# Kernel optimization log

Hardware: AMD Instinct MI355X
Metric: run time of the kernel (lower is better)

## Reference

```python
import math
import jax, jax.numpy as jnp
import numpy as np

B, L, D_MODEL = 2, 2048, 768
H = 12            # num_heads == num_key_value_heads
FEAT = 16         # feature_dim
HEAD_DIM = D_MODEL // H  # 64


def taylor_exp(x):
    """Taylor-exp feature map: phi(x) = [1, x/rrd, (x (x) x)/(sqrt(2)*rd)].
    x: [..., d] -> [..., 1 + d + d^2]"""
    d = x.shape[-1]
    rd = math.sqrt(d)
    rrd = math.sqrt(rd)
    r2 = math.sqrt(2.0)
    x2 = (x[..., :, None] * x[..., None, :]).reshape(*x.shape[:-1], d * d) / r2
    ones = jnp.ones(x.shape[:-1] + (1,), dtype=x.dtype)
    return jnp.concatenate([ones, x / rrd, x2 / rd], axis=-1)


def setup_inputs() -> dict:
    key = jax.random.key(0)
    k1, k2, k3, k4, k5 = jax.random.split(key, 5)
    s = 0.02
    return {
        "hidden_states": jax.random.normal(k1, (B, L, D_MODEL), jnp.float32),
        "Wq": jax.random.normal(k2, (H * FEAT, D_MODEL), jnp.float32) * s,
        "Wk": jax.random.normal(k3, (H * FEAT, D_MODEL), jnp.float32) * s,
        "Wv": jax.random.normal(k4, (D_MODEL, D_MODEL), jnp.float32) * s,
        "Wo": jax.random.normal(k5, (D_MODEL, D_MODEL), jnp.float32) * s,
    }


def reference(hidden_states, Wq, Wk, Wv, Wo):
    b, l, d = hidden_states.shape
    # projections (torch Linear, no bias): y = x @ W.T
    q = jnp.einsum('bld,fd->blf', hidden_states, Wq).reshape(b, l, H, FEAT).transpose(0, 2, 1, 3)
    k = jnp.einsum('bld,fd->blf', hidden_states, Wk).reshape(b, l, H, FEAT).transpose(0, 2, 1, 3)
    v = jnp.einsum('bld,fd->blf', hidden_states, Wv).reshape(b, l, H, HEAD_DIM).transpose(0, 2, 1, 3)

    q = taylor_exp(q)   # [b,h,l,Dexp]
    k = taylor_exp(k)   # k_enc == k (forward clones k), v_enc == v

    # denominator: k_enc.sum over seq + causal cumsum of k
    k_state = jnp.sum(k, axis=2, keepdims=True) + jnp.cumsum(k, axis=2)  # [b,h,l,Dexp]
    z = 1.0 / jnp.sum(q * k_state, axis=-1)                              # [b,h,l]

    # quadratic scores; y1 uses causal (tril) mask, y2 uses full scores with same k,v
    A = jnp.einsum('bhnd,bhmd->bhnm', q, k)                              # [b,h,l,l]
    causal = jnp.tril(jnp.ones((l, l), dtype=A.dtype))
    A_total = A * causal + A                                             # tril(A) + A
    y = jnp.einsum('bhnm,bhme->bhne', A_total, v) * z[..., None]         # [b,h,l,e]

    out = y.transpose(0, 2, 1, 3).reshape(b, l, H * HEAD_DIM)
    return jnp.einsum('blf,df->bld', out, Wo)
```

## Files before the change

kernel.cpp:

```cpp
#include <hip/hip_runtime.h>

typedef unsigned short ushortT;
typedef __bf16 bf16x8 __attribute__((ext_vector_type(8)));
typedef float f32x4 __attribute__((ext_vector_type(4)));

#define BB   2
#define LL   2048
#define DM   768
#define HH   12
#define FT   16
#define HD   64
#define DEXP 273
#define CH   128
#define NC   16
#define NBH  24
#define NBLK 384
#define C2f  0.17677669529663687f
#define KH   768
#define KP   1536
#define SLAB_US   4096
#define SPK_BLK_US 36864
#define SPK_BLK_B  73728

__device__ __forceinline__ void split_bf16(float x, ushortT& hi, ushortT& lo) {
  unsigned b = __float_as_uint(x);
  unsigned r = b + 0x7FFFu + ((b >> 16) & 1u);
  hi = (ushortT)(r >> 16);
  float hf = __uint_as_float((unsigned)hi << 16);
  lo = (ushortT)(__float_as_uint(x - hf) >> 16);
}

__global__ __launch_bounds__(256) void pack_a(const float* __restrict__ X,
                                              ushortT* __restrict__ Xh,
                                              int total4) {
  int g = blockIdx.x * 256 + threadIdx.x;
  if (g >= total4) return;
  int m = g / 192, k4 = (g % 192) * 4;
  float4 v = *(const float4*)(X + (size_t)m * 768 + k4);
  ushortT h[4], l[4];
  split_bf16(v.x, h[0], l[0]);
  split_bf16(v.y, h[1], l[1]);
  split_bf16(v.z, h[2], l[2]);
  split_bf16(v.w, h[3], l[3]);
  ushortT* p = Xh + (size_t)m * KP + k4;
  *(ushort4*)p = *(ushort4*)h;
  *(ushort4*)(p + KH) = *(ushort4*)l;
}

__global__ __launch_bounds__(256) void pack_w(const float* __restrict__ W0,
                                              const float* __restrict__ W1,
                                              const float* __restrict__ W2,
                                              int n1, int n2,
                                              ushortT* __restrict__ Wh,
                                              int total4) {
  int g = blockIdx.x * 256 + threadIdx.x;
  if (g >= total4) return;
  int n = g / 192, k4 = (g % 192) * 4;
  const float* src = (n < n1 ? W0 + (size_t)n * 768
                    : n < n2 ? W1 + (size_t)(n - n1) * 768
                             : W2 + (size_t)(n - n2) * 768);
  float4 v = *(const float4*)(src + k4);
  ushortT h[4], l[4];
  split_bf16(v.x, h[0], l[0]);
  split_bf16(v.y, h[1], l[1]);
  split_bf16(v.z, h[2], l[2]);
  split_bf16(v.w, h[3], l[3]);
  ushortT* p = Wh + (size_t)n * KP + k4;
  *(ushort4*)p = *(ushort4*)h;
  *(ushort4*)(p + KH) = *(ushort4*)l;
}

typedef const __attribute__((address_space(1))) unsigned gq_t;
typedef __attribute__((address_space(3))) unsigned lq_t;
__device__ __forceinline__ void gload_lds16(const ushortT* g, ushortT* l) {
  __builtin_amdgcn_global_load_lds((gq_t*)g, (lq_t*)l, 16, 0, 0);
}

__global__ __launch_bounds__(256) void mfma_gemm(const ushortT* __restrict__ A,
                                                 const ushortT* __restrict__ B,
                                                 float* __restrict__ Y, int ldy,
                                                 int ntiles) {
  __shared__ ushortT sAh[128 * 32], sAl[128 * 32], sBh[64 * 32], sBl[64 * 32];
  const int blk = blockIdx.x;
  const int xcd = blk & 7, slot = blk >> 3;
  const int mtp = gridDim.x / (8 * ntiles);
  const int mt = xcd * mtp + slot / ntiles;
  const int nt = slot % ntiles;
  const int bm = mt * 128, bn = nt * 64;
  const int tid = threadIdx.x, wave = tid >> 6, lane = tid & 63;
  const int srow = lane >> 2, schk = (lane & 3) * 8;
  const ushortT* gsrc;
  ushortT* lb;
  int iters;
  switch (wave) {
    case 0:  gsrc = A + (size_t)(bm + srow) * KP + schk;      lb = sAh; iters = 8; break;
    case 1:  gsrc = A + (size_t)(bm + srow) * KP + KH + schk; lb = sAl; iters = 8; break;
    case 2:  gsrc = B + (size_t)(bn + srow) * KP + schk;      lb = sBh; iters = 4; break;
    default: gsrc = B + (size_t)(bn + srow) * KP + KH + schk; lb = sBl; iters = 4; break;
  }
  const int wm = (wave & 1) * 64, wn = (wave >> 1) * 32;
  const int fr = lane & 15, quad = lane >> 4;
  f32x4 acc[4][2] = {};
  for (int k0 = 0; k0 < KH; k0 += 32) {
    __syncthreads();
    for (int it = 0; it < iters; it++)
      gload_lds16(gsrc + k0 + (size_t)it * 16 * KP, lb + it * 512);
    __syncthreads();
    bf16x8 ah[4], al[4], bh2[2], bl2[2];
#pragma unroll
    for (int mi = 0; mi < 4; mi++) {
      ah[mi] = *(const bf16x8*)&sAh[(wm + mi * 16 + fr) * 32 + quad * 8];
      al[mi] = *(const bf16x8*)&sAl[(wm + mi * 16 + fr) * 32 + quad * 8];
    }
#pragma unroll
    for (int ni = 0; ni < 2; ni++) {
      bh2[ni] = *(const bf16x8*)&sBh[(wn + ni * 16 + fr) * 32 + quad * 8];
      bl2[ni] = *(const bf16x8*)&sBl[(wn + ni * 16 + fr) * 32 + quad * 8];
    }
#pragma unroll
    for (int mi = 0; mi < 4; mi++)
#pragma unroll
      for (int ni = 0; ni < 2; ni++) {
        acc[mi][ni] = __builtin_amdgcn_mfma_f32_16x16x32_bf16(ah[mi], bh2[ni], acc[mi][ni], 0, 0, 0);
        acc[mi][ni] = __builtin_amdgcn_mfma_f32_16x16x32_bf16(ah[mi], bl2[ni], acc[mi][ni], 0, 0, 0);
        acc[mi][ni] = __builtin_amdgcn_mfma_f32_16x16x32_bf16(al[mi], bh2[ni], acc[mi][ni], 0, 0, 0);
      }
  }
  const int orow = quad * 4;
#pragma unroll
  for (int mi = 0; mi < 4; mi++)
#pragma unroll
    for (int ni = 0; ni < 2; ni++) {
      float* yp = Y + (size_t)(bm + wm + mi * 16 + orow) * ldy + bn + wn + ni * 16 + fr;
#pragma unroll
      for (int r = 0; r < 4; r++) yp[(size_t)r * ldy] = acc[mi][ni][r];
    }
}

__global__ __launch_bounds__(256, 2) void chunk_sum_kernel(
    const float* __restrict__ qkv, ushortT* __restrict__ Spk,
    float* __restrict__ csk) {
  const int blk = blockIdx.x;
  const int bh = blk >> 4, c = blk & 15;
  const int b = bh / HH, h = bh % HH;
  __shared__ float kT[16][128];
  __shared__ ushortT phiA[288][72];
  __shared__ ushortT Vt[64][72];
  const float* base = qkv + (size_t)(b * LL + c * CH) * 1152;
  const int tid = threadIdx.x;
  const int wave = tid >> 6, lane = tid & 63;
  const int fr = lane & 15, quad = lane >> 4;
  for (int idx = tid; idx < 512; idx += 256) {
    int m = idx >> 2, i4 = (idx & 3) * 4;
    float4 k4 = *(const float4*)&base[(size_t)m * 1152 + 192 + h * 16 + i4];
    kT[i4 + 0][m] = k4.x; kT[i4 + 1][m] = k4.y;
    kT[i4 + 2][m] = k4.z; kT[i4 + 3][m] = k4.w;
  }
  const int wm2 = (wave & 1) * 144, wn2 = (wave >> 1) * 32;
  f32x4 acc[9][2] = {};
  __syncthreads();
#pragma unroll 1
  for (int s = 0; s < 4; s++) {
    const int m0 = s * 32;
    if (s) __syncthreads();
    for (int idx = tid; idx < 512; idx += 256) {
      int m = m0 + (idx >> 4), e4 = (idx & 15) * 4;
      float4 v4 = *(const float4*)&base[(size_t)m * 1152 + 384 + h * 64 + e4];
      ushortT hh[4], ll[4];
      split_bf16(v4.x, hh[0], ll[0]); split_bf16(v4.y, hh[1], ll[1]);
      split_bf16(v4.z, hh[2], ll[2]); split_bf16(v4.w, hh[3], ll[3]);
      const int mi2 = m - m0;
#pragma unroll
      for (int j = 0; j < 4; j++) {
        Vt[e4 + j][mi2] = hh[j];
        Vt[e4 + j][32 + mi2] = ll[j];
      }
    }
    for (int rr = tid; rr < 288; rr += 256) {
      const int f = rr;
      const float* pa = (f >= 17) ? kT[(f - 17) >> 4] : (f >= 1 ? kT[f - 1] : kT[0]);
      const float* pb = (f >= 17) ? kT[(f - 17) & 15] : kT[0];
      const float sc = (f == 0) ? 1.0f : (f < 17 ? 0.5f : C2f);
      const bool quadf = (f >= 17);
      const bool valid = (f < DEXP);
      ushortT hrow[32], lrow[32];
#pragma unroll
      for (int g = 0; g < 8; g++) {
        float4 a4 = *(const float4*)&pa[m0 + g * 4];
        float4 b4 = *(const float4*)&pb[m0 + g * 4];
        float v0, v1, v2, v3;
        if (f == 0) {
          v0 = v1 = v2 = v3 = 1.0f;
        } else if (!quadf) {
          v0 = sc * a4.x; v1 = sc * a4.y; v2 = sc * a4.z; v3 = sc * a4.w;
        } else {
          v0 = sc * a4.x * b4.x; v1 = sc * a4.y * b4.y;
          v2 = sc * a4.z * b4.z; v3 = sc * a4.w * b4.w;
        }
        if (!valid) { v0 = v1 = v2 = v3 = 0.0f; }
        split_bf16(v0, hrow[g * 4 + 0], lrow[g * 4 + 0]);
        split_bf16(v1, hrow[g * 4 + 1], lrow[g * 4 + 1]);
        split_bf16(v2, hrow[g * 4 + 2], lrow[g * 4 + 2]);
        split_bf16(v3, hrow[g * 4 + 3], lrow[g * 4 + 3]);
      }
      *(uint4*)&phiA[f][0] = *(uint4*)&hrow[0];
      *(uint4*)&phiA[f][8] = *(uint4*)&hrow[8];
      *(uint4*)&phiA[f][16] = *(uint4*)&hrow[16];
      *(uint4*)&phiA[f][24] = *(uint4*)&hrow[24];
      *(uint4*)&phiA[f][32] = *(uint4*)&lrow[0];
      *(uint4*)&phiA[f][40] = *(uint4*)&lrow[8];
      *(uint4*)&phiA[f][48] = *(uint4*)&lrow[16];
      *(uint4*)&phiA[f][56] = *(uint4*)&lrow[24];
    }
    __syncthreads();
    bf16x8 bhf[2], blf[2];
#pragma unroll
    for (int ni = 0; ni < 2; ni++) {
      bhf[ni] = *(const bf16x8*)&Vt[wn2 + ni * 16 + fr][quad * 8];
      blf[ni] = *(const bf16x8*)&Vt[wn2 + ni * 16 + fr][32 + quad * 8];
    }
#pragma unroll
    for (int mi = 0; mi < 9; mi++) {
      bf16x8 ah = *(const bf16x8*)&phiA[wm2 + mi * 16 + fr][quad * 8];
      bf16x8 al = *(const bf16x8*)&phiA[wm2 + mi * 16 + fr][32 + quad * 8];
#pragma unroll
      for (int ni = 0; ni < 2; ni++) {
        acc[mi][ni] = __builtin_amdgcn_mfma_f32_16x16x32_bf16(ah, bhf[ni], acc[mi][ni], 0, 0, 0);
        acc[mi][ni] = __builtin_amdgcn_mfma_f32_16x16x32_bf16(ah, blf[ni], acc[mi][ni], 0, 0, 0);
        acc[mi][ni] = __builtin_amdgcn_mfma_f32_16x16x32_bf16(al, bhf[ni], acc[mi][ni], 0, 0, 0);
      }
    }
  }
  for (int f = tid; f < DEXP; f += 256) {
    float sum = 0.0f;
    if (f == 0) {
      sum = (float)CH;
    } else if (f < 17) {
      const float* p = kT[f - 1];
      for (int m = 0; m < CH; m += 4) {
        float4 x = *(const float4*)&p[m];
        sum += x.x + x.y + x.z + x.w;
      }
      sum *= 0.5f;
    } else {
      const float* pa2 = kT[(f - 17) >> 4];
      const float* pb2 = kT[(f - 17) & 15];
      for (int m = 0; m < CH; m += 4) {
        float4 x = *(const float4*)&pa2[m];
        float4 y = *(const float4*)&pb2[m];
        sum += x.x * y.x + x.y * y.y + x.z * y.z + x.w * y.w;
      }
      sum *= C2f;
    }
    csk[(size_t)blk * DEXP + f] = sum;
  }
  __syncthreads();
  ushortT* stage = &phiA[0][0];
  ushortT* Sp = Spk + (size_t)blk * SPK_BLK_US;
#pragma unroll 1
  for (int sl = 0; sl < 9; sl++) {
    if (sl) __syncthreads();
#pragma unroll
    for (int mi = 0; mi < 9; mi++) {
      const int fb = wm2 + mi * 16;
      if ((fb >> 5) == sl) {
        const int fi0 = (fb & 31) + quad * 4;
        const int gh = fi0 >> 3;
        const int inner = (fi0 << 1) & 15;
#pragma unroll
        for (int ni = 0; ni < 2; ni++) {
          const int e = wn2 + ni * 16 + fr;
          const int es = (e & 7) << 4;
          ushortT hh2[4], ll2[4];
#pragma unroll
          for (int r = 0; r < 4; r++) split_bf16(acc[mi][ni][r], hh2[r], ll2[r]);
          char* rowp = (char*)stage + e * 128;
          *(ushort4*)(rowp + ((gh << 4) ^ es) + inner) = *(ushort4*)hh2;
          *(ushort4*)(rowp + (((gh + 4) << 4) ^ es) + inner) = *(ushort4*)ll2;
        }
      }
    }
    __syncthreads();
    uint4* gdst = (uint4*)(Sp + (size_t)sl * SLAB_US);
    const uint4* lsrc = (const uint4*)stage;
    gdst[tid] = lsrc[tid];
    gdst[tid + 256] = lsrc[tid + 256];
  }
}

__global__ __launch_bounds__(256) void prefix_kernel(ushortT* __restrict__ Spk,
                                                     float* __restrict__ csk) {
  const int gid = blockIdx.x * 256 + threadIdx.x;
  const int totS = NBH * 4608;
  if (gid < totS) {
    const int bh = gid / 4608;
    const int rem = gid % 4608;
    const int slab = rem >> 9;
    const int e = (rem >> 3) & 63;
    const int wp = rem & 7;
    const int es = (e & 7) << 4;
    const unsigned off_h = e * 128 + ((((wp >> 1)) << 4) ^ es) + ((wp & 1) << 3);
    const unsigned off_l = e * 128 + ((((wp >> 1) + 4) << 4) ^ es) + ((wp & 1) << 3);
    char* base = (char*)Spk + (size_t)bh * NC * SPK_BLK_B + slab * 8192;
    float r0[NC], r1[NC], r2[NC], r3[NC];
    float t0 = 0.f, t1 = 0.f, t2 = 0.f, t3 = 0.f;
#pragma unroll
    for (int cc = 0; cc < NC; cc++) {
      const char* p = base + (size_t)cc * SPK_BLK_B;
      ushort4 hw = *(const ushort4*)(p + off_h);
      ushort4 lw = *(const ushort4*)(p + off_l);
      r0[cc] = __uint_as_float((unsigned)hw.x << 16) + __uint_as_float((unsigned)lw.x << 16);
      r1[cc] = __uint_as_float((unsigned)hw.y << 16) + __uint_as_float((unsigned)lw.y << 16);
      r2[cc] = __uint_as_float((unsigned)hw.z << 16) + __uint_as_float((unsigned)lw.z << 16);
      r3[cc] = __uint_as_float((unsigned)hw.w << 16) + __uint_as_float((unsigned)lw.w << 16);
      t0 += r0[cc]; t1 += r1[cc]; t2 += r2[cc]; t3 += r3[cc];
    }
    float u0 = 0.f, u1 = 0.f, u2 = 0.f, u3 = 0.f;
#pragma unroll
    for (int cc = 0; cc < NC; cc++) {
      ushort4 hw, lw;
      split_bf16(u0 + t0, hw.x, lw.x);
      split_bf16(u1 + t1, hw.y, lw.y);
      split_bf16(u2 + t2, hw.z, lw.z);
      split_bf16(u3 + t3, hw.w, lw.w);
      char* p = base + (size_t)cc * SPK_BLK_B;
      *(ushort4*)(p + off_h) = hw;
      *(ushort4*)(p + off_l) = lw;
      u0 += r0[cc]; u1 += r1[cc]; u2 += r2[cc]; u3 += r3[cc];
    }
  } else {
    const int g2 = gid - totS;
    if (g2 < NBH * DEXP) {
      const int bh = g2 / DEXP;
      const int f = g2 % DEXP;
      float r[NC];
      float tot = 0.0f;
#pragma unroll
      for (int cc = 0; cc < NC; cc++) {
        r[cc] = csk[(size_t)(bh * NC + cc) * DEXP + f];
        tot += r[cc];
      }
      float run = 0.0f;
#pragma unroll
      for (int cc = 0; cc < NC; cc++) {
        csk[(size_t)(bh * NC + cc) * DEXP + f] = run + tot;
        run += r[cc];
      }
    }
  }
}

__global__ __launch_bounds__(256, 2) void fused_out(
    const float* __restrict__ qkv, const ushortT* __restrict__ Spk,
    const float* __restrict__ csk, ushortT* __restrict__ Ahat) {
  const int blk = blockIdx.x;
  const int bh = blk >> 4, c = blk & 15;
  const int b = bh / HH, h = bh % HH;
  __shared__ ushortT phiA[128][72];
  __shared__ ushortT GtD[2][4096];
  __shared__ ushortT qA1[128][40];
  __shared__ ushortT qA2[128][40];
  __shared__ ushortT kB[32][40];
  __shared__ ushortT onesB[16][72];
  __shared__ float dred[128][2];
  __shared__ float zl[128];
  const int tid = threadIdx.x;
  const int wv = tid >> 6, lane = tid & 63;
  const int fr = lane & 15, quad = lane >> 4;
  const int prow = tid >> 1, phalf = tid & 1;
  const float* base = qkv + (size_t)(b * LL + c * CH) * 1152;
  const float* qrow = base + (size_t)prow * 1152 + h * 16;
  const ushortT* Gp = Spk + (size_t)blk * SPK_BLK_US;
  float qr[16];
#pragma unroll
  for (int i = 0; i < 4; i++) {
    float4 v = *(const float4*)(qrow + i * 4);
    qr[i * 4 + 0] = v.x; qr[i * 4 + 1] = v.y;
    qr[i * 4 + 2] = v.z; qr[i * 4 + 3] = v.w;
  }
  {
    const ushortT* s0 = Gp + wv * 1024 + lane * 8;
    gload_lds16(s0, &GtD[0][wv * 1024]);
    gload_lds16(s0 + 512, &GtD[0][wv * 1024 + 512]);
  }
  {
    ushortT qh[16], ql[16];
#pragma unroll
    for (int i = 0; i < 16; i++) split_bf16(qr[i], qh[i], ql[i]);
    *(uint4*)&qA1[prow][phalf * 16] = *(uint4*)&qh[0];
    *(uint4*)&qA1[prow][phalf * 16 + 8] = *(uint4*)&qh[8];
    *(uint4*)&qA2[prow][phalf * 16] = *(uint4*)&ql[0];
    *(uint4*)&qA2[prow][phalf * 16 + 8] = *(uint4*)&ql[8];
  }
  for (int idx = tid; idx < 16 * 64; idx += 256) {
    int row = idx >> 6, k = idx & 63;
    onesB[row][k] = (row == 0 && k < 32) ? (ushortT)0x3F80 : (ushortT)0;
  }
  const float* gkp = csk + (size_t)blk * DEXP;
  f32x4 acc[2][5] = {};
  float dacc = 0.0f;
#pragma unroll 1
  for (int s = 0; s < 9; s++) {
    __syncthreads();
    const int f0 = s * 32;
    float gkv[16];
#pragma unroll
    for (int j = 0; j < 16; j++) {
      const int f = f0 + phalf * 16 + j;
      gkv[j] = (f < DEXP) ? gkp[f] : 0.0f;
    }
    __builtin_amdgcn_sched_barrier(0);
    if (s < 8) {
      const ushortT* src = Gp + (s + 1) * SLAB_US + wv * 1024 + lane * 8;
      gload_lds16(src, &GtD[(s + 1) & 1][wv * 1024]);
      gload_lds16(src + 512, &GtD[(s + 1) & 1][wv * 1024 + 512]);
    }
    {
      ushortT h16[16], l16[16];
#pragma unroll
      for (int j = 0; j < 16; j++) {
        const int f = f0 + phalf * 16 + j;
        float v;
        if (f == 0) v = 1.0f;
        else if (f < 17) v = 0.5f * qr[f - 1];
        else if (f < DEXP) {
          const int ii = f - 17;
          v = C2f * qr[ii >> 4] * qr[ii & 15];
        } else v = 0.0f;
        dacc += v * gkv[j];
        split_bf16(v, h16[j], l16[j]);
      }
      *(uint4*)&phiA[prow][phalf * 16] = *(uint4*)&h16[0];
      *(uint4*)&phiA[prow][phalf * 16 + 8] = *(uint4*)&h16[8];
      *(uint4*)&phiA[prow][32 + phalf * 16] = *(uint4*)&l16[0];
      *(uint4*)&phiA[prow][32 + phalf * 16 + 8] = *(uint4*)&l16[8];
    }
    bf16x8 ah[2], al[2];
#pragma unroll
    for (int mi = 0; mi < 2; mi++) {
      ah[mi] = *(const bf16x8*)&phiA[wv * 32 + mi * 16 + fr][quad * 8];
      al[mi] = *(const bf16x8*)&phiA[wv * 32 + mi * 16 + fr][32 + quad * 8];
    }
    const char* gt = (const char*)&GtD[s & 1][0];
    const int sw = (fr & 7) << 4;
#pragma unroll
    for (int ni = 0; ni < 4; ni++) {
      const int rb = (ni * 16 + fr) * 128;
      bf16x8 bh2 = *(const bf16x8*)(gt + rb + ((quad * 16) ^ sw));
      bf16x8 bl2 = *(const bf16x8*)(gt + rb + ((64 + quad * 16) ^ sw));
#pragma unroll
      for (int mi = 0; mi < 2; mi++) {
        acc[mi][ni] = __builtin_amdgcn_mfma_f32_16x16x32_bf16(ah[mi], bh2, acc[mi][ni], 0, 0, 0);
        acc[mi][ni] = __builtin_amdgcn_mfma_f32_16x16x32_bf16(ah[mi], bl2, acc[mi][ni], 0, 0, 0);
        acc[mi][ni] = __builtin_amdgcn_mfma_f32_16x16x32_bf16(al[mi], bh2, acc[mi][ni], 0, 0, 0);
      }
    }
  }
  dred[prow][phalf] = dacc;
  __syncthreads();
  ushortT* VtF = &GtD[0][0];
#pragma unroll 1
  for (int s = 0; s < 4; s++) {
    const int m0 = s * 32;
    for (int idx = tid; idx < 128; idx += 256) {
      int mL = idx >> 2, i4 = (idx & 3) * 4;
      float4 k4 = *(const float4*)&base[(size_t)(m0 + mL) * 1152 + 192 + h * 16 + i4];
      ushortT hh[4], ll[4];
      split_bf16(k4.x, hh[0], ll[0]); split_bf16(k4.y, hh[1], ll[1]);
      split_bf16(k4.z, hh[2], ll[2]); split_bf16(k4.w, hh[3], ll[3]);
      *(ushort4*)&kB[mL][i4] = *(ushort4*)hh;
      *(ushort4*)&kB[mL][16 + i4] = *(ushort4*)ll;
    }
    for (int idx = tid; idx < 512; idx += 256) {
      int mL = idx >> 4, e4 = (idx & 15) * 4;
      float4 v4 = *(const float4*)&base[(size_t)(m0 + mL) * 1152 + 384 + h * 64 + e4];
      ushortT hh[4], ll[4];
      split_bf16(v4.x, hh[0], ll[0]); split_bf16(v4.y, hh[1], ll[1]);
      split_bf16(v4.z, hh[2], ll[2]); split_bf16(v4.w, hh[3], ll[3]);
#pragma unroll
      for (int j = 0; j < 4; j++) {
        VtF[(e4 + j) * 72 + mL] = hh[j];
        VtF[(e4 + j) * 72 + 32 + mL] = ll[j];
      }
    }
    __syncthreads();
    if (s <= wv) {
#pragma unroll
      for (int rt = 0; rt < 2; rt++) {
        bf16x8 a1 = *(const bf16x8*)&qA1[wv * 32 + rt * 16 + fr][quad * 8];
        bf16x8 a2 = *(const bf16x8*)&qA2[wv * 32 + rt * 16 + fr][quad * 8];
#pragma unroll
        for (int mtt = 0; mtt < 2; mtt++) {
          bf16x8 bk = *(const bf16x8*)&kB[mtt * 16 + fr][quad * 8];
          f32x4 sf = {};
          sf = __builtin_amdgcn_mfma_f32_16x16x32_bf16(a1, bk, sf, 0, 0, 0);
          sf = __builtin_amdgcn_mfma_f32_16x16x32_bf16(a2, bk, sf, 0, 0, 0);
          const int mg = m0 + mtt * 16 + fr;
#pragma unroll
          for (int r = 0; r < 4; r++) {
            const int rowL = wv * 32 + rt * 16 + quad * 4 + r;
            const float sv = sf[r];
            const float p = (mg <= rowL) ? fmaf(sv, fmaf(sv, 0.03125f, 0.25f), 1.0f) : 0.0f;
            ushortT ph, pl;
            split_bf16(p, ph, pl);
            phiA[rowL][mtt * 16 + fr] = ph;
            phiA[rowL][32 + mtt * 16 + fr] = pl;
          }
        }
      }
#pragma unroll
      for (int mi = 0; mi < 2; mi++) {
        bf16x8 ah = *(const bf16x8*)&phiA[wv * 32 + mi * 16 + fr][quad * 8];
        bf16x8 al = *(const bf16x8*)&phiA[wv * 32 + mi * 16 + fr][32 + quad * 8];
#pragma unroll
        for (int ni = 0; ni < 5; ni++) {
          bf16x8 bh2 = (ni < 4) ? *(const bf16x8*)&VtF[(ni * 16 + fr) * 72 + quad * 8]
                                : *(const bf16x8*)&onesB[fr][quad * 8];
          bf16x8 bl2 = (ni < 4) ? *(const bf16x8*)&VtF[(ni * 16 + fr) * 72 + 32 + quad * 8]
                                : *(const bf16x8*)&onesB[fr][32 + quad * 8];
          acc[mi][ni] = __builtin_amdgcn_mfma_f32_16x16x32_bf16(ah, bh2, acc[mi][ni], 0, 0, 0);
          acc[mi][ni] = __builtin_amdgcn_mfma_f32_16x16x32_bf16(ah, bl2, acc[mi][ni], 0, 0, 0);
          acc[mi][ni] = __builtin_amdgcn_mfma_f32_16x16x32_bf16(al, bh2, acc[mi][ni], 0, 0, 0);
        }
      }
    }
    __syncthreads();
  }
  if (fr == 0) {
#pragma unroll
    for (int mi = 0; mi < 2; mi++)
#pragma unroll
      for (int r = 0; r < 4; r++) {
        const int rowL = wv * 32 + mi * 16 + quad * 4 + r;
        const float d = dred[rowL][0] + dred[rowL][1] + acc[mi][4][r];
        zl[rowL] = 1.0f / d;
      }
  }
  __syncthreads();
  const size_t rowbase = (size_t)(b * LL + c * CH);
#pragma unroll
  for (int mi = 0; mi < 2; mi++)
#pragma unroll
    for (int ni = 0; ni < 4; ni++)
#pragma unroll
      for (int r = 0; r < 4; r++) {
        const int rowL = wv * 32 + mi * 16 + quad * 4 + r;
        const float val = acc[mi][ni][r] * zl[rowL];
        ushortT hh, ll;
        split_bf16(val, hh, ll);
        ushortT* ap = Ahat + (rowbase + rowL) * (size_t)KP + h * 64 + ni * 16 + fr;
        ap[0] = hh;
        ap[KH] = ll;
      }
}

extern "C" void kernel_launch(void* const* d_in, const int* in_sizes, int n_in,
                              void* d_out, int out_size, void* d_ws, size_t ws_size,
                              hipStream_t stream) {
  const float* hs = (const float*)d_in[0];
  const float* Wq = (const float*)d_in[1];
  const float* Wk = (const float*)d_in[2];
  const float* Wv = (const float*)d_in[3];
  const float* Wo = (const float*)d_in[4];
  float* out = (float*)d_out;
  char* ws = (char*)d_ws;
  float* qkv = (float*)(ws);
  char*  attR = ws + 18874368;
  ushortT* Spk = (ushortT*)(ws + 31457280);
  float* csk = (float*)(ws + 59768832);
  ushortT* Xhat = (ushortT*)(ws + 31457280);
  ushortT* What = (ushortT*)attR;
  ushortT* Ahat = (ushortT*)attR;
  ushortT* Wohat = (ushortT*)qkv;
  const dim3 thr(256);
  pack_a<<<3072, thr, 0, stream>>>(hs, Xhat, 4096 * 192);
  pack_w<<<864, thr, 0, stream>>>(Wq, Wk, Wv, 192, 384, What, 1152 * 192);
  mfma_gemm<<<576, thr, 0, stream>>>(Xhat, What, qkv, 1152, 18);
  chunk_sum_kernel<<<NBLK, thr, 0, stream>>>(qkv, Spk, csk);
  {
    const int tot = NBH * 4608 + NBH * DEXP;
    prefix_kernel<<<(tot + 255) / 256, thr, 0, stream>>>(Spk, csk);
  }
  fused_out<<<NBLK, thr, 0, stream>>>(qkv, Spk, csk, Ahat);
  pack_w<<<576, thr, 0, stream>>>(Wo, Wo, Wo, 768, 768, Wohat, 768 * 192);
  mfma_gemm<<<384, thr, 0, stream>>>(Ahat, Wohat, out, DM, 12);
}
```

Baseline: 246.6 us.

## Double fused_out block to 512 threads and fold denominator dot into MFMA

The fused_out kernel now runs 8 waves of 16 rows each instead of 4 waves of 32 rows, halving per-thread accumulator state and phi-building work per thread. The scalar denominator dot product against the cumulative key sum is replaced by an extra MFMA column that uses bf16-split gk values staged in shared memory, and the ones-column MFMA is trimmed. This raises parallelism per block and removes the dred reduction. The causal chunk loop still idles half the waves on early slabs, and the gk term now goes through a bf16 hi/lo split with the lo*lo product dropped, which slightly changes precision.

```diff
diff --git a/kernel.cpp b/kernel.cpp
--- a/kernel.cpp
+++ b/kernel.cpp
@@ -350,7 +350,7 @@
   }
 }
 
-__global__ __launch_bounds__(256, 2) void fused_out(
+__global__ __launch_bounds__(512, 4) void fused_out(
     const float* __restrict__ qkv, const ushortT* __restrict__ Spk,
     const float* __restrict__ csk, ushortT* __restrict__ Ahat) {
   const int blk = blockIdx.x;
@@ -358,16 +358,17 @@
   const int b = bh / HH, h = bh % HH;
   __shared__ ushortT phiA[128][72];
   __shared__ ushortT GtD[2][4096];
-  __shared__ ushortT qA1[128][40];
-  __shared__ ushortT qA2[128][40];
+  __shared__ ushortT qA1[128][24];
+  __shared__ ushortT qA2[128][24];
   __shared__ ushortT kB[32][40];
-  __shared__ ushortT onesB[16][72];
-  __shared__ float dred[128][2];
+  __shared__ ushortT gkS[9][64];
+  __shared__ ushortT zero64[64];
+  __shared__ ushortT onesRow[64];
   __shared__ float zl[128];
   const int tid = threadIdx.x;
   const int wv = tid >> 6, lane = tid & 63;
   const int fr = lane & 15, quad = lane >> 4;
-  const int prow = tid >> 1, phalf = tid & 1;
+  const int prow = tid >> 2, pq = tid & 3;
   const float* base = qkv + (size_t)(b * LL + c * CH) * 1152;
   const float* qrow = base + (size_t)prow * 1152 + h * 16;
   const ushortT* Gp = Spk + (size_t)blk * SPK_BLK_US;
@@ -378,48 +379,41 @@
     qr[i * 4 + 0] = v.x; qr[i * 4 + 1] = v.y;
     qr[i * 4 + 2] = v.z; qr[i * 4 + 3] = v.w;
   }
+  gload_lds16(Gp + wv * 512 + lane * 8, &GtD[0][wv * 512]);
   {
-    const ushortT* s0 = Gp + wv * 1024 + lane * 8;
-    gload_lds16(s0, &GtD[0][wv * 1024]);
-    gload_lds16(s0 + 512, &GtD[0][wv * 1024 + 512]);
+    ushortT qh4[4], ql4[4];
+#pragma unroll
+    for (int i = 0; i < 4; i++) split_bf16(qr[pq * 4 + i], qh4[i], ql4[i]);
+    *(ushort4*)&qA1[prow][pq * 4] = *(ushort4*)qh4;
+    *(ushort4*)&qA2[prow][pq * 4] = *(ushort4*)ql4;
   }
   {
-    ushortT qh[16], ql[16];
-#pragma unroll
-    for (int i = 0; i < 16; i++) split_bf16(qr[i], qh[i], ql[i]);
-    *(uint4*)&qA1[prow][phalf * 16] = *(uint4*)&qh[0];
-    *(uint4*)&qA1[prow][phalf * 16 + 8] = *(uint4*)&qh[8];
-    *(uint4*)&qA2[prow][phalf * 16] = *(uint4*)&ql[0];
-    *(uint4*)&qA2[prow][phalf * 16 + 8] = *(uint4*)&ql[8];
-  }
-  for (int idx = tid; idx < 16 * 64; idx += 256) {
-    int row = idx >> 6, k = idx & 63;
-    onesB[row][k] = (row == 0 && k < 32) ? (ushortT)0x3F80 : (ushortT)0;
-  }
-  const float* gkp = csk + (size_t)blk * DEXP;
-  f32x4 acc[2][5] = {};
-  float dacc = 0.0f;
+    const float* gkp = csk + (size_t)blk * DEXP;
+    for (int f = tid; f < 288; f += 512) {
+      float v = (f < DEXP) ? gkp[f] : 0.0f;
+      ushortT hh, ll;
+      split_bf16(v, hh, ll);
+      gkS[f >> 5][f & 31] = hh;
+      gkS[f >> 5][32 + (f & 31)] = ll;
+    }
+  }
+  if (tid < 64) {
+    zero64[tid] = 0;
+    onesRow[tid] = (tid < 32) ? (ushortT)0x3F80 : (ushortT)0;
+  }
+  f32x4 acc[5] = {};
 #pragma unroll 1
   for (int s = 0; s < 9; s++) {
     __syncthreads();
+    if (s < 8)
+      gload_lds16(Gp + (s + 1) * SLAB_US + wv * 512 + lane * 8,
+                  &GtD[(s + 1) & 1][wv * 512]);
     const int f0 = s * 32;
-    float gkv[16];
-#pragma unroll
-    for (int j = 0; j < 16; j++) {
-      const int f = f0 + phalf * 16 + j;
-      gkv[j] = (f < DEXP) ? gkp[f] : 0.0f;
-    }
-    __builtin_amdgcn_sched_barrier(0);
-    if (s < 8) {
-      const ushortT* src = Gp + (s + 1) * SLAB_US + wv * 1024 + lane * 8;
-      gload_lds16(src, &GtD[(s + 1) & 1][wv * 1024]);
-      gload_lds16(src + 512, &GtD[(s + 1) & 1][wv * 1024 + 512]);
-    }
     {
-      ushortT h16[16], l16[16];
-#pragma unroll
-      for (int j = 0; j < 16; j++) {
-        const int f = f0 + phalf * 16 + j;
+      ushortT h8[8], l8[8];
+#pragma unroll
+      for (int j = 0; j < 8; j++) {
+        const int f = f0 + pq * 8 + j;
         float v;
         if (f == 0) v = 1.0f;
         else if (f < 17) v = 0.5f * qr[f - 1];
@@ -427,20 +421,13 @@
           const int ii = f - 17;
           v = C2f * qr[ii >> 4] * qr[ii & 15];
         } else v = 0.0f;
-        dacc += v * gkv[j];
-        split_bf16(v, h16[j], l16[j]);
-      }
-      *(uint4*)&phiA[prow][phalf * 16] = *(uint4*)&h16[0];
-      *(uint4*)&phiA[prow][phalf * 16 + 8] = *(uint4*)&h16[8];
-      *(uint4*)&phiA[prow][32 + phalf * 16] = *(uint4*)&l16[0];
-      *(uint4*)&phiA[prow][32 + phalf * 16 + 8] = *(uint4*)&l16[8];
-    }
-    bf16x8 ah[2], al[2];
-#pragma unroll
-    for (int mi = 0; mi < 2; mi++) {
-      ah[mi] = *(const bf16x8*)&phiA[wv * 32 + mi * 16 + fr][quad * 8];
-      al[mi] = *(const bf16x8*)&phiA[wv * 32 + mi * 16 + fr][32 + quad * 8];
-    }
+        split_bf16(v, h8[j], l8[j]);
+      }
+      *(uint4*)&phiA[prow][pq * 8] = *(uint4*)&h8[0];
+      *(uint4*)&phiA[prow][32 + pq * 8] = *(uint4*)&l8[0];
+    }
+    bf16x8 ah = *(const bf16x8*)&phiA[wv * 16 + fr][quad * 8];
+    bf16x8 al = *(const bf16x8*)&phiA[wv * 16 + fr][32 + quad * 8];
     const char* gt = (const char*)&GtD[s & 1][0];
     const int sw = (fr & 7) << 4;
 #pragma unroll
@@ -448,22 +435,26 @@
       const int rb = (ni * 16 + fr) * 128;
       bf16x8 bh2 = *(const bf16x8*)(gt + rb + ((quad * 16) ^ sw));
       bf16x8 bl2 = *(const bf16x8*)(gt + rb + ((64 + quad * 16) ^ sw));
-#pragma unroll
-      for (int mi = 0; mi < 2; mi++) {
-        acc[mi][ni] = __builtin_amdgcn_mfma_f32_16x16x32_bf16(ah[mi], bh2, acc[mi][ni], 0, 0, 0);
-        acc[mi][ni] = __builtin_amdgcn_mfma_f32_16x16x32_bf16(ah[mi], bl2, acc[mi][ni], 0, 0, 0);
-        acc[mi][ni] = __builtin_amdgcn_mfma_f32_16x16x32_bf16(al[mi], bh2, acc[mi][ni], 0, 0, 0);
-      }
-    }
-  }
-  dred[prow][phalf] = dacc;
+      acc[ni] = __builtin_amdgcn_mfma_f32_16x16x32_bf16(ah, bh2, acc[ni], 0, 0, 0);
+      acc[ni] = __builtin_amdgcn_mfma_f32_16x16x32_bf16(ah, bl2, acc[ni], 0, 0, 0);
+      acc[ni] = __builtin_amdgcn_mfma_f32_16x16x32_bf16(al, bh2, acc[ni], 0, 0, 0);
+    }
+    {
+      const ushortT* gp = (fr == 0) ? &gkS[s][0] : &zero64[0];
+      bf16x8 gh = *(const bf16x8*)(gp + quad * 8);
+      bf16x8 gl = *(const bf16x8*)(gp + 32 + quad * 8);
+      acc[4] = __builtin_amdgcn_mfma_f32_16x16x32_bf16(ah, gh, acc[4], 0, 0, 0);
+      acc[4] = __builtin_amdgcn_mfma_f32_16x16x32_bf16(ah, gl, acc[4], 0, 0, 0);
+      acc[4] = __builtin_amdgcn_mfma_f32_16x16x32_bf16(al, gh, acc[4], 0, 0, 0);
+    }
+  }
   __syncthreads();
   ushortT* VtF = &GtD[0][0];
 #pragma unroll 1
   for (int s = 0; s < 4; s++) {
     const int m0 = s * 32;
-    for (int idx = tid; idx < 128; idx += 256) {
-      int mL = idx >> 2, i4 = (idx & 3) * 4;
+    if (tid < 128) {
+      int mL = tid >> 2, i4 = (tid & 3) * 4;
       float4 k4 = *(const float4*)&base[(size_t)(m0 + mL) * 1152 + 192 + h * 16 + i4];
       ushortT hh[4], ll[4];
       split_bf16(k4.x, hh[0], ll[0]); split_bf16(k4.y, hh[1], ll[1]);
@@ -471,8 +462,8 @@
       *(ushort4*)&kB[mL][i4] = *(ushort4*)hh;
       *(ushort4*)&kB[mL][16 + i4] = *(ushort4*)ll;
     }
-    for (int idx = tid; idx < 512; idx += 256) {
-      int mL = idx >> 4, e4 = (idx & 15) * 4;
+    {
+      int mL = tid >> 4, e4 = (tid & 15) * 4;
       float4 v4 = *(const float4*)&base[(size_t)(m0 + mL) * 1152 + 384 + h * 64 + e4];
       ushortT hh[4], ll[4];
       split_bf16(v4.x, hh[0], ll[0]); split_bf16(v4.y, hh[1], ll[1]);
@@ -484,74 +475,66 @@
       }
     }
     __syncthreads();
-    if (s <= wv) {
-#pragma unroll
-      for (int rt = 0; rt < 2; rt++) {
-        bf16x8 a1 = *(const bf16x8*)&qA1[wv * 32 + rt * 16 + fr][quad * 8];
-        bf16x8 a2 = *(const bf16x8*)&qA2[wv * 32 + rt * 16 + fr][quad * 8];
-#pragma unroll
-        for (int mtt = 0; mtt < 2; mtt++) {
-          bf16x8 bk = *(const bf16x8*)&kB[mtt * 16 + fr][quad * 8];
-          f32x4 sf = {};
-          sf = __builtin_amdgcn_mfma_f32_16x16x32_bf16(a1, bk, sf, 0, 0, 0);
-          sf = __builtin_amdgcn_mfma_f32_16x16x32_bf16(a2, bk, sf, 0, 0, 0);
-          const int mg = m0 + mtt * 16 + fr;
-#pragma unroll
-          for (int r = 0; r < 4; r++) {
-            const int rowL = wv * 32 + rt * 16 + quad * 4 + r;
-            const float sv = sf[r];
-            const float p = (mg <= rowL) ? fmaf(sv, fmaf(sv, 0.03125f, 0.25f), 1.0f) : 0.0f;
-            ushortT ph, pl;
-            split_bf16(p, ph, pl);
-            phiA[rowL][mtt * 16 + fr] = ph;
-            phiA[rowL][32 + mtt * 16 + fr] = pl;
-          }
+    if (s <= (wv >> 1)) {
+      bf16x8 a1 = *(const bf16x8*)&qA1[wv * 16 + fr][(quad & 1) * 8];
+      bf16x8 a2 = *(const bf16x8*)&qA2[wv * 16 + fr][(quad & 1) * 8];
+#pragma unroll
+      for (int mtt = 0; mtt < 2; mtt++) {
+        bf16x8 bk = *(const bf16x8*)&kB[mtt * 16 + fr][quad * 8];
+        f32x4 sf = {};
+        sf = __builtin_amdgcn_mfma_f32_16x16x32_bf16(a1, bk, sf, 0, 0, 0);
+        sf = __builtin_amdgcn_mfma_f32_16x16x32_bf16(a2, bk, sf, 0, 0, 0);
+        const int mg = m0 + mtt * 16 + fr;
+#pragma unroll
+        for (int r = 0; r < 4; r++) {
+          const int rowL = wv * 16 + quad * 4 + r;
+          const float sv = sf[r];
+          const float p = (mg <= rowL) ? fmaf(sv, fmaf(sv, 0.03125f, 0.25f), 1.0f) : 0.0f;
+          ushortT ph, pl;
+          split_bf16(p, ph, pl);
+          phiA[rowL][mtt * 16 + fr] = ph;
+          phiA[rowL][32 + mtt * 16 + fr] = pl;
         }
       }
-#pragma unroll
-      for (int mi = 0; mi < 2; mi++) {
-        bf16x8 ah = *(const bf16x8*)&phiA[wv * 32 + mi * 16 + fr][quad * 8];
-        bf16x8 al = *(const bf16x8*)&phiA[wv * 32 + mi * 16 + fr][32 + quad * 8];
-#pragma unroll
-        for (int ni = 0; ni < 5; ni++) {
-          bf16x8 bh2 = (ni < 4) ? *(const bf16x8*)&VtF[(ni * 16 + fr) * 72 + quad * 8]
-                                : *(const bf16x8*)&onesB[fr][quad * 8];
-          bf16x8 bl2 = (ni < 4) ? *(const bf16x8*)&VtF[(ni * 16 + fr) * 72 + 32 + quad * 8]
-                                : *(const bf16x8*)&onesB[fr][32 + quad * 8];
-          acc[mi][ni] = __builtin_amdgcn_mfma_f32_16x16x32_bf16(ah, bh2, acc[mi][ni], 0, 0, 0);
-          acc[mi][ni] = __builtin_amdgcn_mfma_f32_16x16x32_bf16(ah, bl2, acc[mi][ni], 0, 0, 0);
-          acc[mi][ni] = __builtin_amdgcn_mfma_f32_16x16x32_bf16(al, bh2, acc[mi][ni], 0, 0, 0);
-        }
+      bf16x8 ah = *(const bf16x8*)&phiA[wv * 16 + fr][quad * 8];
+      bf16x8 al = *(const bf16x8*)&phiA[wv * 16 + fr][32 + quad * 8];
+#pragma unroll
+      for (int ni = 0; ni < 4; ni++) {
+        bf16x8 bh2 = *(const bf16x8*)&VtF[(ni * 16 + fr) * 72 + quad * 8];
+        bf16x8 bl2 = *(const bf16x8*)&VtF[(ni * 16 + fr) * 72 + 32 + quad * 8];
+        acc[ni] = __builtin_amdgcn_mfma_f32_16x16x32_bf16(ah, bh2, acc[ni], 0, 0, 0);
+        acc[ni] = __builtin_amdgcn_mfma_f32_16x16x32_bf16(ah, bl2, acc[ni], 0, 0, 0);
+        acc[ni] = __builtin_amdgcn_mfma_f32_16x16x32_bf16(al, bh2, acc[ni], 0, 0, 0);
+      }
+      {
+        const ushortT* op = (fr == 0) ? &onesRow[0] : &zero64[0];
+        bf16x8 oh = *(const bf16x8*)(op + quad * 8);
+        acc[4] = __builtin_amdgcn_mfma_f32_16x16x32_bf16(ah, oh, acc[4], 0, 0, 0);
+        acc[4] = __builtin_amdgcn_mfma_f32_16x16x32_bf16(al, oh, acc[4], 0, 0, 0);
       }
     }
     __syncthreads();
   }
   if (fr == 0) {
 #pragma unroll
-    for (int mi = 0; mi < 2; mi++)
-#pragma unroll
-      for (int r = 0; r < 4; r++) {
-        const int rowL = wv * 32 + mi * 16 + quad * 4 + r;
-        const float d = dred[rowL][0] + dred[rowL][1] + acc[mi][4][r];
-        zl[rowL] = 1.0f / d;
-      }
-  }
-  __syncthreads();
+    for (int r = 0; r < 4; r++) {
+      const int rowL = wv * 16 + quad * 4 + r;
+      zl[rowL] = 1.0f / acc[4][r];
+    }
+  }
   const size_t rowbase = (size_t)(b * LL + c * CH);
 #pragma unroll
-  for (int mi = 0; mi < 2; mi++)
-#pragma unroll
-    for (int ni = 0; ni < 4; ni++)
-#pragma unroll
-      for (int r = 0; r < 4; r++) {
-        const int rowL = wv * 32 + mi * 16 + quad * 4 + r;
-        const float val = acc[mi][ni][r] * zl[rowL];
-        ushortT hh, ll;
-        split_bf16(val, hh, ll);
-        ushortT* ap = Ahat + (rowbase + rowL) * (size_t)KP + h * 64 + ni * 16 + fr;
-        ap[0] = hh;
-        ap[KH] = ll;
-      }
+  for (int ni = 0; ni < 4; ni++)
+#pragma unroll
+    for (int r = 0; r < 4; r++) {
+      const int rowL = wv * 16 + quad * 4 + r;
+      const float val = acc[ni][r] * zl[rowL];
+      ushortT hh, ll;
+      split_bf16(val, hh, ll);
+      ushortT* ap = Ahat + (rowbase + rowL) * (size_t)KP + h * 64 + ni * 16 + fr;
+      ap[0] = hh;
+      ap[KH] = ll;
+    }
 }
 
 extern "C" void kernel_launch(void* const* d_in, const int* in_sizes, int n_in,
@@ -581,7 +564,7 @@
     const int tot = NBH * 4608 + NBH * DEXP;
     prefix_kernel<<<(tot + 255) / 256, thr, 0, stream>>>(Spk, csk);
   }
-  fused_out<<<NBLK, thr, 0, stream>>>(qkv, Spk, csk, Ahat);
+  fused_out<<<NBLK, dim3(512), 0, stream>>>(qkv, Spk, csk, Ahat);
   pack_w<<<576, thr, 0, stream>>>(Wo, Wo, Wo, 768, 768, Wohat, 768 * 192);
   mfma_gemm<<<384, thr, 0, stream>>>(Ahat, Wohat, out, DM, 12);
 }
```

Result: no change. 244.4 us (-0.9%).
